# Kernel optimization log

Hardware: AMD Instinct MI355X
Metric: run time of the kernel (lower is better)

Reference implementation:

```python
import jax, jax.numpy as jnp
import numpy as np

N_NODES = 50000


def _gcn_conv(x, edge_index, W, b):
    # PyG GCNConv (default flags): add self-loops, symmetric normalization,
    # linear transform, scatter-add aggregation, bias.
    N = x.shape[0]
    row, col = edge_index[0], edge_index[1]  # messages flow row -> col
    loop = jnp.arange(N)
    row_f = jnp.concatenate([row, loop])
    col_f = jnp.concatenate([col, loop])
    deg = jax.ops.segment_sum(jnp.ones(col_f.shape[0], dtype=x.dtype), col_f,
                              num_segments=N)
    deg_inv_sqrt = jnp.where(deg > 0, jax.lax.rsqrt(jnp.maximum(deg, 1e-12)), 0.0)
    norm = deg_inv_sqrt[row_f] * deg_inv_sqrt[col_f]  # [E+N]
    h = x @ W                                          # [N, out]
    msg = h[row_f] * norm[:, None]                     # gather + scale
    out = jax.ops.segment_sum(msg, col_f, num_segments=N)  # scatter-add
    return out + b


def setup_inputs() -> dict:
    key = jax.random.key(0)
    ks = jax.random.split(key, 6)
    d_in, d_hid, d_out = 128, 128, 64
    E = 800000
    x = jax.random.normal(ks[0], (N_NODES, d_in), dtype=jnp.float32)
    edge_index = jax.random.randint(ks[1], (2, E), 0, N_NODES, dtype=jnp.int64)
    edge_label = jax.random.uniform(ks[2], (100000,), dtype=jnp.float32)
    edge_label_index = jax.random.randint(ks[3], (2, 100000), 0, N_NODES,
                                          dtype=jnp.int64)
    # Glorot-style init for GCNConv linear weights
    W1 = jax.random.normal(ks[4], (d_in, d_hid), dtype=jnp.float32) / np.sqrt(d_in)
    b1 = jnp.zeros((d_hid,), dtype=jnp.float32)
    W2 = jax.random.normal(ks[5], (d_hid, d_out), dtype=jnp.float32) / np.sqrt(d_hid)
    b2 = jnp.zeros((d_out,), dtype=jnp.float32)
    return {"x": x, "edge_index": edge_index, "edge_label": edge_label,
            "edge_label_index": edge_label_index,
            "W1": W1, "b1": b1, "W2": W2, "b2": b2}


def reference(x, edge_index, edge_label, edge_label_index, W1, b1, W2, b2):
    h = jax.nn.relu(_gcn_conv(x, edge_index, W1, b1))
    # dropout is identity in eval mode (training=False)
    z = _gcn_conv(h, edge_index, W2, b2)
    return z
```

## Files before the change

### kernel.cpp

```cpp
#include <hip/hip_runtime.h>


typedef unsigned int u32;
typedef unsigned short ushort;
typedef __attribute__((ext_vector_type(8))) short short8;
typedef __attribute__((ext_vector_type(4))) float floatx4;

static inline int cdiv_l(long a, int b) { return (int)((a + b - 1) / b); }

constexpr int NPB  = 512;
constexpr int EPB  = 4096;
constexpr int MAXB = 128;
constexpr int CAP  = 12288;

__device__ __forceinline__ u32 pack_bf16(float a, float b) {
  union { float f; u32 i; } ua, ub;
  ua.f = a; ub.f = b;
  u32 x = (ua.i + 0x7fffu + ((ua.i >> 16) & 1u)) >> 16;
  u32 y = (ub.i + 0x7fffu + ((ub.i >> 16) & 1u)) & 0xffff0000u;
  return x | y;
}

__device__ __forceinline__ short bf16r(float f) {
  union { float f; u32 i; } u; u.f = f;
  return (short)((u.i + 0x7fffu + ((u.i >> 16) & 1u)) >> 16);
}

__device__ __forceinline__ void add8(float* a, uint4 v) {
  union { u32 i; float f; } t;
  t.i = v.x << 16;         a[0] += t.f;
  t.i = v.x & 0xffff0000u; a[1] += t.f;
  t.i = v.y << 16;         a[2] += t.f;
  t.i = v.y & 0xffff0000u; a[3] += t.f;
  t.i = v.z << 16;         a[4] += t.f;
  t.i = v.z & 0xffff0000u; a[5] += t.f;
  t.i = v.w << 16;         a[6] += t.f;
  t.i = v.w & 0xffff0000u; a[7] += t.f;
}

__device__ __forceinline__ void fma8(float* a, uint4 v, float s) {
  union { u32 i; float f; } t;
  t.i = v.x << 16;         a[0] += t.f * s;
  t.i = v.x & 0xffff0000u; a[1] += t.f * s;
  t.i = v.y << 16;         a[2] += t.f * s;
  t.i = v.y & 0xffff0000u; a[3] += t.f * s;
  t.i = v.z << 16;         a[4] += t.f * s;
  t.i = v.z & 0xffff0000u; a[5] += t.f * s;
  t.i = v.w << 16;         a[6] += t.f * s;
  t.i = v.w & 0xffff0000u; a[7] += t.f * s;
}

__global__ __launch_bounds__(256) void k_fused1(
    const int* __restrict__ ei, int* __restrict__ cur, u32* __restrict__ ebuf,
    int E, int NBE,
    const float* __restrict__ x, const float* __restrict__ W1,
    u32* __restrict__ h, int N) {
  __shared__ float eb[4][16 * 133];
  __shared__ int hist[MAXB];
  __shared__ int curs[MAXB];
  const int tid = threadIdx.x;

  if (blockIdx.x < (unsigned)NBE) {
    const int* ecol = ei + E;
    if (tid < MAXB) hist[tid] = 0;
    __syncthreads();
    const int base = blockIdx.x * EPB;
#pragma unroll
    for (int j = 0; j < EPB / 256; ++j) {
      int e = base + j * 256 + tid;
      if (e < E) atomicAdd(hist + (ecol[e] >> 9), 1);
    }
    __syncthreads();
    if (tid < MAXB) {
      int n = hist[tid];
      curs[tid] = tid * CAP + (n ? atomicAdd(cur + tid, n) : 0);
    }
    __syncthreads();
#pragma unroll
    for (int j = 0; j < EPB / 256; ++j) {
      int e = base + j * 256 + tid;
      if (e < E) {
        int r = ei[e];
        int c = ecol[e];
        int b = c >> 9;
        int p = atomicAdd(curs + b, 1);
        if (p < (b + 1) * CAP)
          ebuf[p] = (u32)r | ((u32)(c & (NPB - 1)) << 16);
      }
    }
    return;
  }

  constexpr int K = 128, M = 128, NC = 8, LROW = 133, WW = 64;
  const int w = tid >> 6, lane = tid & 63;
  const int quad = lane >> 4, n16 = lane & 15;
  const int row0 = ((blockIdx.x - NBE) * 4 + w) * 16;

  floatx4 acc[NC];
#pragma unroll
  for (int c = 0; c < NC; ++c) acc[c] = {0.f, 0.f, 0.f, 0.f};

  const int am = row0 + n16;
  const bool av = am < N;
  const float* arow = x + (long)am * K;

#pragma unroll
  for (int kc = 0; kc < 4; ++kc) {
    const int kb = kc * 32 + quad * 8;
    float4 a0 = make_float4(0.f, 0.f, 0.f, 0.f);
    float4 a1 = make_float4(0.f, 0.f, 0.f, 0.f);
    if (av) {
      a0 = *(const float4*)(arow + kb);
      a1 = *(const float4*)(arow + kb + 4);
    }
    short8 af;
    af[0] = bf16r(a0.x); af[1] = bf16r(a0.y); af[2] = bf16r(a0.z); af[3] = bf16r(a0.w);
    af[4] = bf16r(a1.x); af[5] = bf16r(a1.y); af[6] = bf16r(a1.z); af[7] = bf16r(a1.w);
    const float* wbase = W1 + (long)kb * M + n16;
#pragma unroll
    for (int c = 0; c < NC; ++c) {
      const float* wp = wbase + c * 16;
      short8 bf;
      bf[0] = bf16r(wp[0 * M]); bf[1] = bf16r(wp[1 * M]);
      bf[2] = bf16r(wp[2 * M]); bf[3] = bf16r(wp[3 * M]);
      bf[4] = bf16r(wp[4 * M]); bf[5] = bf16r(wp[5 * M]);
      bf[6] = bf16r(wp[6 * M]); bf[7] = bf16r(wp[7 * M]);
      acc[c] = __builtin_amdgcn_mfma_f32_16x16x32_bf16(af, bf, acc[c], 0, 0, 0);
    }
  }

  float* ep = eb[w];
#pragma unroll
  for (int c = 0; c < NC; ++c)
#pragma unroll
    for (int r = 0; r < 4; ++r)
      ep[(quad * 4 + r) * LROW + c * 16 + n16] = acc[c][r];
  __syncthreads();

#pragma unroll
  for (int i = 0; i < 16 * WW / 64; ++i) {
    int idx = i * 64 + lane;
    int r = idx / WW, cp = idx % WW;
    int rg = row0 + r;
    if (rg < N) {
      u32 p = pack_bf16(ep[r * LROW + 2 * cp], ep[r * LROW + 2 * cp + 1]);
      h[(long)rg * WW + cp] = p;
    }
  }
}

__global__ __launch_bounds__(NPB) void k_csr(const u32* __restrict__ ebuf,
                                             const int* __restrict__ cur,
                                             int* __restrict__ off,
                                             int* __restrict__ deg,
                                             float* __restrict__ dis,
                                             ushort* __restrict__ csr, int N) {
  __shared__ int cnt[NPB];
  __shared__ int curl[NPB];
  __shared__ int wsum[NPB / 64];
  const int tid = threadIdx.x;
  const int b = blockIdx.x;
  const int s = b * CAP;
  const int e = s + min(cur[b], CAP);
  cnt[tid] = 0;
  __syncthreads();
  for (int i = s + tid; i < e; i += NPB)
    atomicAdd(cnt + (ebuf[i] >> 16), 1);
  __syncthreads();
  const int lane = tid & 63, w = tid >> 6;
  int v = cnt[tid];
  int incl = v;
#pragma unroll
  for (int d = 1; d < 64; d <<= 1) {
    int x = __shfl_up(incl, d, 64);
    if (lane >= d) incl += x;
  }
  if (lane == 63) wsum[w] = incl;
  __syncthreads();
  if (w == 0 && lane < NPB / 64) {
    int sv = wsum[lane];
#pragma unroll
    for (int d = 1; d < NPB / 64; d <<= 1) {
      int x = __shfl_up(sv, d, 64);
      if (lane >= d) sv += x;
    }
    wsum[lane] = sv;
  }
  __syncthreads();
  int excl = ((w > 0) ? wsum[w - 1] : 0) + incl - v;
  int node = b * NPB + tid;
  if (node < N) {
    off[node] = s + excl;
    deg[node] = v;
    dis[node] = rsqrtf((float)v + 1.0f);
  }
  curl[tid] = excl;
  __syncthreads();
  for (int i = s + tid; i < e; i += NPB) {
    u32 pk = ebuf[i];
    int p = atomicAdd(curl + (pk >> 16), 1);
    csr[s + p] = (ushort)(pk & 0xffffu);
  }
}

__global__ __launch_bounds__(256) void k_gg(
    const uint4* __restrict__ hs, const int* __restrict__ off,
    const int* __restrict__ deg, const ushort* __restrict__ csr,
    const float* __restrict__ dis, const float* __restrict__ b1,
    const float* __restrict__ W2, u32* __restrict__ h2, int N) {
  constexpr int LG = 65;
  constexpr int LC = 66;
  __shared__ u32 lg[16 * LG];
  __shared__ float cb[16 * LC];
  const int tid = threadIdx.x;
  const int r = tid >> 4;
  const int lf = tid & 15;
  const int row0 = blockIdx.x * 16;
  const int n = row0 + r;

  u32 gw[4] = {0, 0, 0, 0};
  if (n < N) {
    const int s = off[n], e = s + deg[n];
    const float dn = dis[n];
    float acc[8] = {};
    fma8(acc, hs[(long)n * 16 + lf], dn);
    int j = s;
    for (; j + 4 <= e; j += 4) {
      int s0 = csr[j], s1 = csr[j + 1], s2 = csr[j + 2], s3 = csr[j + 3];
      float d0 = dis[s0], d1 = dis[s1], d2 = dis[s2], d3 = dis[s3];
      uint4 v0 = hs[(long)s0 * 16 + lf];
      uint4 v1 = hs[(long)s1 * 16 + lf];
      uint4 v2 = hs[(long)s2 * 16 + lf];
      uint4 v3 = hs[(long)s3 * 16 + lf];
      fma8(acc, v0, d0); fma8(acc, v1, d1); fma8(acc, v2, d2); fma8(acc, v3, d3);
    }
    for (; j < e; ++j) {
      int s0 = csr[j];
      fma8(acc, hs[(long)s0 * 16 + lf], dis[s0]);
    }
    const int f8 = lf * 8;
#pragma unroll
    for (int q = 0; q < 8; ++q)
      acc[q] = fmaxf(acc[q] * dn + b1[f8 + q], 0.f);
#pragma unroll
    for (int q = 0; q < 4; ++q)
      gw[q] = pack_bf16(acc[2 * q], acc[2 * q + 1]);
  }
#pragma unroll
  for (int q = 0; q < 4; ++q) lg[r * LG + lf * 4 + q] = gw[q];
  __syncthreads();

  const int w = tid >> 6, lane = tid & 63;
  const int quad = lane >> 4, n16 = lane & 15;
  floatx4 acc4 = {0.f, 0.f, 0.f, 0.f};
#pragma unroll
  for (int kc = 0; kc < 4; ++kc) {
    const int kb = kc * 32 + quad * 8;
    const u32* ap = &lg[n16 * LG + (kb >> 1)];
    u32 aw[4] = {ap[0], ap[1], ap[2], ap[3]};
    short8 af = *(short8*)aw;
    const float* wp = W2 + (long)kb * 64 + w * 16 + n16;
    short8 bf;
    bf[0] = bf16r(wp[0 * 64]); bf[1] = bf16r(wp[1 * 64]);
    bf[2] = bf16r(wp[2 * 64]); bf[3] = bf16r(wp[3 * 64]);
    bf[4] = bf16r(wp[4 * 64]); bf[5] = bf16r(wp[5 * 64]);
    bf[6] = bf16r(wp[6 * 64]); bf[7] = bf16r(wp[7 * 64]);
    acc4 = __builtin_amdgcn_mfma_f32_16x16x32_bf16(af, bf, acc4, 0, 0, 0);
  }
  float dd[4];
#pragma unroll
  for (int r4 = 0; r4 < 4; ++r4) {
    int rg = row0 + quad * 4 + r4;
    dd[r4] = (rg < N) ? dis[rg] : 0.f;
  }
#pragma unroll
  for (int r4 = 0; r4 < 4; ++r4)
    cb[(quad * 4 + r4) * LC + w * 16 + n16] = acc4[r4] * dd[r4];
  __syncthreads();

#pragma unroll
  for (int i = 0; i < 2; ++i) {
    int idx = i * 256 + tid;
    int rr = idx >> 5, cw = idx & 31;
    int rg = row0 + rr;
    if (rg < N) {
      u32 p = pack_bf16(cb[rr * LC + 2 * cw], cb[rr * LC + 2 * cw + 1]);
      h2[(long)rg * 32 + cw] = p;
    }
  }
}

__global__ __launch_bounds__(256) void k_gather2(
    const uint4* __restrict__ hs, const int* __restrict__ off,
    const int* __restrict__ deg, const ushort* __restrict__ csr,
    const float* __restrict__ dis, const float* __restrict__ bias,
    float* __restrict__ out, int N) {
  constexpr int L = 8;
  const int local = threadIdx.x / L;
  const int lf = threadIdx.x % L;
  const int n = blockIdx.x * (256 / L) + local;
  if (n >= N) return;
  const int s = off[n], e = s + deg[n];
  float acc[8] = {};
  add8(acc, hs[(long)n * L + lf]);
  int j = s;
  for (; j + 4 <= e; j += 4) {
    int s0 = csr[j], s1 = csr[j + 1], s2 = csr[j + 2], s3 = csr[j + 3];
    uint4 v0 = hs[(long)s0 * L + lf];
    uint4 v1 = hs[(long)s1 * L + lf];
    uint4 v2 = hs[(long)s2 * L + lf];
    uint4 v3 = hs[(long)s3 * L + lf];
    add8(acc, v0); add8(acc, v1); add8(acc, v2); add8(acc, v3);
  }
  for (; j < e; ++j) add8(acc, hs[(long)csr[j] * L + lf]);
  const float d = dis[n];
  const int f8 = lf * 8;
  const float4 b0 = *(const float4*)(bias + f8);
  const float4 b1v = *(const float4*)(bias + f8 + 4);
  float4 o0, o1;
  o0.x = acc[0] * d + b0.x;
  o0.y = acc[1] * d + b0.y;
  o0.z = acc[2] * d + b0.z;
  o0.w = acc[3] * d + b0.w;
  o1.x = acc[4] * d + b1v.x;
  o1.y = acc[5] * d + b1v.y;
  o1.z = acc[6] * d + b1v.z;
  o1.w = acc[7] * d + b1v.w;
  *(float4*)(out + (long)n * 64 + f8) = o0;
  *(float4*)(out + (long)n * 64 + f8 + 4) = o1;
}

extern "C" void kernel_launch(void* const* d_in, const int* in_sizes, int n_in,
                              void* d_out, int out_size, void* d_ws, size_t ws_size,
                              hipStream_t stream) {
  const float* x  = (const float*)d_in[0];
  const int*   ei = (const int*)d_in[1];
  const float* W1 = (const float*)d_in[4];
  const float* b1 = (const float*)d_in[5];
  const float* W2 = (const float*)d_in[6];
  const float* b2 = (const float*)d_in[7];
  float* out = (float*)d_out;

  const int N = in_sizes[0] / 128;
  const int E = in_sizes[1] / 2;
  const int NBKT = cdiv_l(N, NPB);
  const int NBE  = cdiv_l(E, EPB);
  const int G1   = cdiv_l(N, 64);

  const long Np = (N + 64) & ~63L;
  const long BW = (long)NBKT * CAP;
  int*    cur  = (int*)d_ws;
  int*    off  = cur + 128;
  int*    deg  = off + Np;
  float*  dis  = (float*)(deg + Np);
  u32*    ebuf = (u32*)(dis + Np);
  ushort* csr  = (ushort*)(ebuf + BW);
  u32*    h    = (u32*)(csr + BW);
  u32*    h2   = h + (long)N * 64;

  hipMemsetAsync(cur, 0, MAXB * sizeof(int), stream);

  k_fused1<<<NBE + G1, 256, 0, stream>>>(ei, cur, ebuf, E, NBE, x, W1, h, N);

  k_csr<<<NBKT, NPB, 0, stream>>>(ebuf, cur, off, deg, dis, csr, N);

  k_gg<<<cdiv_l(N, 16), 256, 0, stream>>>((const uint4*)h, off, deg, csr,
                                          dis, b1, W2, h2, N);

  k_gather2<<<cdiv_l(N, 32), 256, 0, stream>>>((const uint4*)h2, off, deg, csr,
                                               dis, b2, out, N);
}
```

Baseline: 169.3 us.

## Cache packed edges in LDS during binning and lane-sort neighbor indices in gathers

During edge binning, each edge's row and column are packed into a shared-memory cache on the first pass, so the scatter pass no longer re-reads the edge arrays from global memory. In both gather kernels, neighbor indices are loaded cooperatively in chunks of 16 or 8 and sorted across lanes with a bitonic shuffle network, then broadcast. Visiting sources in ascending order within each chunk is meant to improve locality of the feature-row gathers. In exchange, every chunk pays for the shuffle-based sort, and the shared buffer is reused for the edge cache.

```diff
diff --git a/kernel.cpp b/kernel.cpp
--- a/kernel.cpp
+++ b/kernel.cpp
@@ -50,17 +50,33 @@
   t.i = v.w & 0xffff0000u; a[7] += t.f * s;
 }
 
+template <int W>
+__device__ __forceinline__ int lane_sort(int v, int l) {
+#pragma unroll
+  for (int k = 2; k <= W; k <<= 1) {
+#pragma unroll
+    for (int j = k >> 1; j > 0; j >>= 1) {
+      int o = __shfl_xor(v, j, W);
+      bool asc = ((l & k) == 0);
+      bool low = ((l & j) == 0);
+      v = (asc == low) ? min(v, o) : max(v, o);
+    }
+  }
+  return v;
+}
+
 __global__ __launch_bounds__(256) void k_fused1(
     const int* __restrict__ ei, int* __restrict__ cur, u32* __restrict__ ebuf,
     int E, int NBE,
     const float* __restrict__ x, const float* __restrict__ W1,
     u32* __restrict__ h, int N) {
   __shared__ float eb[4][16 * 133];
-  __shared__ int hist[MAXB];
-  __shared__ int curs[MAXB];
   const int tid = threadIdx.x;
 
   if (blockIdx.x < (unsigned)NBE) {
+    u32* ecache = (u32*)&eb[0][0];
+    int* hist   = (int*)&eb[2][0];
+    int* curs   = hist + MAXB;
     const int* ecol = ei + E;
     if (tid < MAXB) hist[tid] = 0;
     __syncthreads();
@@ -68,7 +84,14 @@
 #pragma unroll
     for (int j = 0; j < EPB / 256; ++j) {
       int e = base + j * 256 + tid;
-      if (e < E) atomicAdd(hist + (ecol[e] >> 9), 1);
+      u32 pk = 0xffffffffu;
+      if (e < E) {
+        u32 r = (u32)ei[e];
+        u32 c = (u32)ecol[e];
+        pk = r | (c << 16);
+        atomicAdd(hist + (c >> 9), 1);
+      }
+      ecache[j * 256 + tid] = pk;
     }
     __syncthreads();
     if (tid < MAXB) {
@@ -78,14 +101,13 @@
     __syncthreads();
 #pragma unroll
     for (int j = 0; j < EPB / 256; ++j) {
-      int e = base + j * 256 + tid;
-      if (e < E) {
-        int r = ei[e];
-        int c = ecol[e];
+      u32 pk = ecache[j * 256 + tid];
+      if (pk != 0xffffffffu) {
+        u32 c = pk >> 16;
         int b = c >> 9;
         int p = atomicAdd(curs + b, 1);
         if (p < (b + 1) * CAP)
-          ebuf[p] = (u32)r | ((u32)(c & (NPB - 1)) << 16);
+          ebuf[p] = (pk & 0xffffu) | ((c & (NPB - 1)) << 16);
       }
     }
     return;
@@ -224,19 +246,28 @@
     const float dn = dis[n];
     float acc[8] = {};
     fma8(acc, hs[(long)n * 16 + lf], dn);
-    int j = s;
-    for (; j + 4 <= e; j += 4) {
-      int s0 = csr[j], s1 = csr[j + 1], s2 = csr[j + 2], s3 = csr[j + 3];
-      float d0 = dis[s0], d1 = dis[s1], d2 = dis[s2], d3 = dis[s3];
-      uint4 v0 = hs[(long)s0 * 16 + lf];
-      uint4 v1 = hs[(long)s1 * 16 + lf];
-      uint4 v2 = hs[(long)s2 * 16 + lf];
-      uint4 v3 = hs[(long)s3 * 16 + lf];
-      fma8(acc, v0, d0); fma8(acc, v1, d1); fma8(acc, v2, d2); fma8(acc, v3, d3);
-    }
-    for (; j < e; ++j) {
-      int s0 = csr[j];
-      fma8(acc, hs[(long)s0 * 16 + lf], dis[s0]);
+    for (int j = s; j < e; j += 16) {
+      int idx = j + lf;
+      int cs = (idx < e) ? (int)csr[idx] : 0x7fffffff;
+      cs = lane_sort<16>(cs, lf);
+      const int cnt = min(e - j, 16);
+      int t = 0;
+      for (; t + 4 <= cnt; t += 4) {
+        int s0 = __shfl(cs, t, 16);
+        int s1 = __shfl(cs, t + 1, 16);
+        int s2 = __shfl(cs, t + 2, 16);
+        int s3 = __shfl(cs, t + 3, 16);
+        float d0 = dis[s0], d1 = dis[s1], d2 = dis[s2], d3 = dis[s3];
+        uint4 v0 = hs[(long)s0 * 16 + lf];
+        uint4 v1 = hs[(long)s1 * 16 + lf];
+        uint4 v2 = hs[(long)s2 * 16 + lf];
+        uint4 v3 = hs[(long)s3 * 16 + lf];
+        fma8(acc, v0, d0); fma8(acc, v1, d1); fma8(acc, v2, d2); fma8(acc, v3, d3);
+      }
+      for (; t < cnt; ++t) {
+        int s0 = __shfl(cs, t, 16);
+        fma8(acc, hs[(long)s0 * 16 + lf], dis[s0]);
+      }
     }
     const int f8 = lf * 8;
 #pragma unroll
@@ -303,16 +334,28 @@
   const int s = off[n], e = s + deg[n];
   float acc[8] = {};
   add8(acc, hs[(long)n * L + lf]);
-  int j = s;
-  for (; j + 4 <= e; j += 4) {
-    int s0 = csr[j], s1 = csr[j + 1], s2 = csr[j + 2], s3 = csr[j + 3];
-    uint4 v0 = hs[(long)s0 * L + lf];
-    uint4 v1 = hs[(long)s1 * L + lf];
-    uint4 v2 = hs[(long)s2 * L + lf];
-    uint4 v3 = hs[(long)s3 * L + lf];
-    add8(acc, v0); add8(acc, v1); add8(acc, v2); add8(acc, v3);
-  }
-  for (; j < e; ++j) add8(acc, hs[(long)csr[j] * L + lf]);
+  for (int j = s; j < e; j += 8) {
+    int idx = j + lf;
+    int cs = (idx < e) ? (int)csr[idx] : 0x7fffffff;
+    cs = lane_sort<8>(cs, lf);
+    const int cnt = min(e - j, 8);
+    int t = 0;
+    for (; t + 4 <= cnt; t += 4) {
+      int s0 = __shfl(cs, t, 8);
+      int s1 = __shfl(cs, t + 1, 8);
+      int s2 = __shfl(cs, t + 2, 8);
+      int s3 = __shfl(cs, t + 3, 8);
+      uint4 v0 = hs[(long)s0 * L + lf];
+      uint4 v1 = hs[(long)s1 * L + lf];
+      uint4 v2 = hs[(long)s2 * L + lf];
+      uint4 v3 = hs[(long)s3 * L + lf];
+      add8(acc, v0); add8(acc, v1); add8(acc, v2); add8(acc, v3);
+    }
+    for (; t < cnt; ++t) {
+      int s0 = __shfl(cs, t, 8);
+      add8(acc, hs[(long)s0 * L + lf]);
+    }
+  }
   const float d = dis[n];
   const int f8 = lf * 8;
   const float4 b0 = *(const float4*)(bias + f8);
```

Result: no change. 167.6 us (-1.0%).
